# Kernel tuning notes

Hardware: AMD Instinct MI355X
Metric: run time of the kernel (lower is better)

The kernel has to match this reference:

```python
import jax, jax.numpy as jnp
import numpy as np

B, S, HID = 4, 2048, 1024
NH = 16
HD = HID // NH  # 64


def setup_inputs() -> dict:
    key = jax.random.key(0)
    k1, k2, k3 = jax.random.split(key, 3)
    x = jax.random.normal(k1, (B, S, HID), dtype=jnp.float32)
    # causal sparse mask: True = attend
    mask = jnp.tril(jnp.ones((S, S), dtype=bool))
    w_qkv = jax.random.normal(k2, (HID, 3 * HID), dtype=jnp.float32) * 0.02
    b_qkv = jnp.zeros((3 * HID,), dtype=jnp.float32)
    w_out = jax.random.normal(k3, (HID, HID), dtype=jnp.float32) * 0.02
    b_out = jnp.zeros((HID,), dtype=jnp.float32)
    return {"x": x, "mask": mask, "w_qkv": w_qkv, "b_qkv": b_qkv,
            "w_out": w_out, "b_out": b_out}


def reference(x, mask, w_qkv, b_qkv, w_out, b_out):
    bsz, seq_len, hid = x.shape
    # QKV projection -> [B, S, H, 3*D] -> [B, H, S, 3*D]
    qkv = (x @ w_qkv + b_qkv).reshape(bsz, seq_len, NH, 3 * HD).transpose(0, 2, 1, 3)
    q, k, v = jnp.split(qkv, 3, axis=-1)  # each [B, H, S, D]
    scale = 1.0 / jnp.sqrt(jnp.asarray(HD, dtype=x.dtype))
    scores = jnp.einsum('bhqd,bhkd->bhqk', q, k) * scale
    scores = jnp.where(mask[None, None, :, :], scores, jnp.asarray(-jnp.inf, dtype=scores.dtype))
    probs = jax.nn.softmax(scores, axis=-1)
    context = jnp.einsum('bhqk,bhkd->bhqd', probs, v)  # [B, H, S, D]
    context = context.transpose(0, 2, 1, 3).reshape(bsz, seq_len, hid)
    return context @ w_out + b_out
```

## Files before the change

kernel.cpp:

```cpp
#include <hip/hip_runtime.h>
#include <stdint.h>

#define S_LEN 2048
#define NHEAD 16
#define HDIM  64
#define HIDDEN 1024
#define BATCH 4

typedef float f32x4 __attribute__((ext_vector_type(4)));
typedef __bf16 bf16x8 __attribute__((ext_vector_type(8)));
typedef unsigned short u16;

union U4B8 { uint4 u; bf16x8 b; };

__device__ __forceinline__ bf16x8 as_b8(uint4 u){ U4B8 x; x.u = u; return x.b; }

__device__ __forceinline__ f32x4 mfma16(uint4 a, uint4 b, f32x4 c){
  return __builtin_amdgcn_mfma_f32_16x16x32_bf16(as_b8(a), as_b8(b), c, 0, 0, 0);
}

__device__ __forceinline__ u16 f2bf(float f){
  __bf16 h = (__bf16)f;
  return __builtin_bit_cast(u16, h);
}

__device__ __forceinline__ float exp2fast(float x){
  return __builtin_exp2f(x);
}

__device__ __forceinline__ void gload16(const void* g, void* l){
  __builtin_amdgcn_global_load_lds(
      (const __attribute__((address_space(1))) unsigned int*)g,
      (__attribute__((address_space(3))) unsigned int*)l, 16, 0, 0);
}

#define QSCALE 0.18033688f
#define DEFER_THR 11.5f

__global__ __launch_bounds__(256) void k_cvt(const float* __restrict__ in,
                                             u16* __restrict__ out, int n4){
  int i = blockIdx.x * 256 + threadIdx.x;
  int stride = gridDim.x * 256;
  for (; i < n4; i += stride){
    float4 v = ((const float4*)in)[i];
    unsigned lo = (unsigned)f2bf(v.x) | ((unsigned)f2bf(v.y) << 16);
    unsigned hi = (unsigned)f2bf(v.z) | ((unsigned)f2bf(v.w) << 16);
    ((uint2*)out)[i] = make_uint2(lo, hi);
  }
}

__global__ __launch_bounds__(256) void k_transpose(const float* __restrict__ in,
                                                   u16* __restrict__ out,
                                                   int K, int N){
  __shared__ float t[32][33];
  int tx = threadIdx.x & 31, ty = threadIdx.x >> 5;
  int n0 = blockIdx.x * 32, k0 = blockIdx.y * 32;
  #pragma unroll
  for (int i = 0; i < 4; ++i)
    t[ty + i*8][tx] = in[(size_t)(k0 + ty + i*8) * N + n0 + tx];
  __syncthreads();
  #pragma unroll
  for (int i = 0; i < 4; ++i)
    out[(size_t)(n0 + ty + i*8) * K + k0 + tx] = f2bf(t[tx][ty + i*8]);
}

__device__ __forceinline__ void stage_gemm(
    const u16* __restrict__ A, const u16* __restrict__ Bt,
    u16* As, u16* Bs, int row0, int col0, int K, int k0, int wave, int lane)
{
  #pragma unroll
  for (int p = 0; p < 2; ++p){
    int chunk = wave * 128 + p * 64 + lane;
    int r = chunk >> 2, cseg = chunk & 3;
    const u16* ga = A  + (size_t)(row0 + r) * K + k0 + cseg * 8;
    gload16(ga, As + (size_t)(wave * 128 + p * 64) * 8);
    const u16* gb = Bt + (size_t)(col0 + r) * K + k0 + cseg * 8;
    gload16(gb, Bs + (size_t)(wave * 128 + p * 64) * 8);
  }
}

template<int MODE>
__global__ __launch_bounds__(256) void k_gemm(
    const u16* __restrict__ A, const u16* __restrict__ Bt,
    const float* __restrict__ bias,
    u16* __restrict__ oq, u16* __restrict__ ok, u16* __restrict__ ov,
    float* __restrict__ of, int M, int N, int K)
{
  __shared__ u16 As[2][128 * 32];
  __shared__ u16 Bs[2][128 * 32];
  const int tid  = threadIdx.x;
  const int wave = tid >> 6, lane = tid & 63;
  const int l4 = lane >> 4, lm = lane & 15;
  const int wr = wave >> 1, wc = wave & 1;
  const int row0 = blockIdx.y * 128;
  const int col0 = blockIdx.x * 128;

  const f32x4 fzero = {0.f, 0.f, 0.f, 0.f};
  f32x4 acc[4][4];
  #pragma unroll
  for (int m = 0; m < 4; ++m)
    #pragma unroll
    for (int n = 0; n < 4; ++n) acc[m][n] = fzero;

  stage_gemm(A, Bt, &As[0][0], &Bs[0][0], row0, col0, K, 0, wave, lane);

  const int nks = K >> 5;
  #pragma unroll 1
  for (int ks = 0; ks < nks; ++ks){
    const int cur = ks & 1;
    if (ks + 1 < nks){
      stage_gemm(A, Bt, &As[cur ^ 1][0], &Bs[cur ^ 1][0],
                 row0, col0, K, (ks + 1) << 5, wave, lane);
      asm volatile("s_waitcnt vmcnt(4)" ::: "memory");
    } else {
      asm volatile("s_waitcnt vmcnt(0)" ::: "memory");
    }
    __builtin_amdgcn_s_barrier();
    asm volatile("" ::: "memory");

    uint4 af[4], bf[4];
    #pragma unroll
    for (int m = 0; m < 4; ++m)
      af[m] = *(const uint4*)&As[cur][(wr * 64 + m * 16 + lm) * 32 + l4 * 8];
    #pragma unroll
    for (int n = 0; n < 4; ++n)
      bf[n] = *(const uint4*)&Bs[cur][(wc * 64 + n * 16 + lm) * 32 + l4 * 8];
    __builtin_amdgcn_s_setprio(1);
    #pragma unroll
    for (int m = 0; m < 4; ++m)
      #pragma unroll
      for (int n = 0; n < 4; ++n)
        acc[m][n] = mfma16(af[m], bf[n], acc[m][n]);
    __builtin_amdgcn_s_setprio(0);

    asm volatile("" ::: "memory");
    __builtin_amdgcn_s_barrier();
    asm volatile("" ::: "memory");
  }

  #pragma unroll
  for (int m = 0; m < 4; ++m){
    #pragma unroll
    for (int n = 0; n < 4; ++n){
      int c = col0 + wc * 64 + n * 16 + lm;
      float bv = bias[c];
      #pragma unroll
      for (int r = 0; r < 4; ++r){
        int row = row0 + wr * 64 + m * 16 + l4 * 4 + r;
        float val = acc[m][n][r] + bv;
        if (MODE == 0){
          int h = c / 192, e = c % 192;
          int which = e >> 6, d = e & 63;
          int b = row >> 11, s = row & 2047;
          int bh = b * 16 + h;
          if (which == 2){
            ov[((size_t)bh * HDIM + d) * S_LEN + s] = f2bf(val);
          } else {
            if (which == 0) val *= QSCALE;
            size_t idx = ((size_t)bh * S_LEN + s) * HDIM + d;
            u16* dst = (which == 0) ? oq : ok;
            dst[idx] = f2bf(val);
          }
        } else {
          of[(size_t)row * N + c] = val;
        }
      }
    }
  }
}

__device__ __forceinline__ void stage_tile(
    const u16* __restrict__ kB, const u16* __restrict__ vB,
    u16* ldsK, u16* ldsV, int kbase, int wave, int lane)
{
  #pragma unroll
  for (int p = 0; p < 2; ++p){
    int ch  = wave * 128 + p * 64 + lane;
    int row = ch >> 3;
    int cc  = (ch & 7) << 4;
    int sc  = cc ^ ((row & 7) << 4);
    const u16* gk = kB + (size_t)(kbase + row) * HDIM + (sc >> 1);
    gload16(gk, ldsK + (size_t)(wave * 128 + p * 64) * 8);
    const u16* gv = vB + (size_t)row * S_LEN + kbase + (sc >> 1);
    gload16(gv, ldsV + (size_t)(wave * 128 + p * 64) * 8);
  }
}

__global__ __launch_bounds__(256) void k_attn(
    const u16* __restrict__ q, const u16* __restrict__ kk,
    const u16* __restrict__ vt, u16* __restrict__ ctx)
{
  __shared__ u16 KV[2][2][64 * 64];
  __shared__ u16 Ps[4][2][16][72];

  const int bid = blockIdx.x;
  const int bh = bid & 63;
  const int pr = bid >> 6;
  const int wave = threadIdx.x >> 6, lane = threadIdx.x & 63;
  const int l4 = lane >> 4, lm = lane & 15;
  const size_t base = (size_t)bh * (S_LEN * HDIM);
  const u16* kB = kk + base;
  const u16* vB = vt + base;
  const int b = bh >> 4, h = bh & 15;
  const f32x4 fz = {0.f, 0.f, 0.f, 0.f};

  #pragma unroll 1
  for (int half = 0; half < 2; ++half){
    const int st = half ? (15 - pr) : pr;
    const int q0 = st * 128 + wave * 32;

    uint4 qf[2][2];
    #pragma unroll
    for (int f = 0; f < 2; ++f){
      const u16* qr = q + base + (size_t)(q0 + f * 16 + lm) * HDIM + l4 * 8;
      qf[f][0] = *(const uint4*)qr;
      qf[f][1] = *(const uint4*)(qr + 32);
    }

    float mr[2] = {-1e30f, -1e30f}, lsp[2] = {0.f, 0.f};
    f32x4 acc[2][4];
    #pragma unroll
    for (int f = 0; f < 2; ++f)
      #pragma unroll
      for (int tt = 0; tt < 4; ++tt) acc[f][tt] = fz;

    const int nkt = 2 * st + 2;

    stage_tile(kB, vB, &KV[0][0][0], &KV[0][1][0], 0, wave, lane);

    #pragma unroll 1
    for (int kt = 0; kt < nkt; ++kt){
      const int cur = kt & 1;
      const int kbase = kt << 6;
      if (kt + 1 < nkt){
        stage_tile(kB, vB, &KV[cur ^ 1][0][0], &KV[cur ^ 1][1][0],
                   (kt + 1) << 6, wave, lane);
        asm volatile("s_waitcnt vmcnt(4)" ::: "memory");
      } else {
        asm volatile("s_waitcnt vmcnt(0)" ::: "memory");
      }
      __builtin_amdgcn_s_barrier();
      asm volatile("" ::: "memory");

      if (kbase < q0 + 32){
        const u16* ldsK = &KV[cur][0][0];
        const u16* ldsV = &KV[cur][1][0];

        f32x4 sv[2][4];
        __builtin_amdgcn_s_setprio(1);
        #pragma unroll
        for (int g = 0; g < 4; ++g){
          int rk = g * 16 + lm;
          int xa = (l4 * 16) ^ ((rk & 7) << 4);
          int xb = (64 + l4 * 16) ^ ((rk & 7) << 4);
          const u16* krow = ldsK + rk * 64;
          uint4 kf0 = *(const uint4*)(krow + (xa >> 1));
          uint4 kf1 = *(const uint4*)(krow + (xb >> 1));
          sv[0][g] = mfma16(kf0, qf[0][0], fz);
          sv[0][g] = mfma16(kf1, qf[0][1], sv[0][g]);
          sv[1][g] = mfma16(kf0, qf[1][0], fz);
          sv[1][g] = mfma16(kf1, qf[1][1], sv[1][g]);
        }
        __builtin_amdgcn_s_setprio(0);

        const bool tail = (kbase + 63 > q0);

        #pragma unroll
        for (int f = 0; f < 2; ++f){
          if (tail){
            #pragma unroll
            for (int g = 0; g < 4; ++g)
              #pragma unroll
              for (int r = 0; r < 4; ++r){
                int kg = kbase + g * 16 + l4 * 4 + r;
                int qg = q0 + f * 16 + lm;
                if (kg > qg) sv[f][g][r] = -1e30f;
              }
          }

          float pm = sv[f][0][0];
          #pragma unroll
          for (int g = 0; g < 4; ++g)
            #pragma unroll
            for (int r = 0; r < 4; ++r) pm = fmaxf(pm, sv[f][g][r]);
          pm = fmaxf(pm, __shfl_xor(pm, 16));
          pm = fmaxf(pm, __shfl_xor(pm, 32));

          if (__any(pm > mr[f] + DEFER_THR)){
            float mn = fmaxf(mr[f], pm);
            float corr = exp2fast(mr[f] - mn);
            mr[f] = mn;
            lsp[f] *= corr;
            float cf[4];
            #pragma unroll
            for (int r = 0; r < 4; ++r) cf[r] = __shfl(corr, l4 * 4 + r);
            #pragma unroll
            for (int tt = 0; tt < 4; ++tt)
              #pragma unroll
              for (int r = 0; r < 4; ++r) acc[f][tt][r] *= cf[r];
          }

          float s_ = 0.f;
          #pragma unroll
          for (int g = 0; g < 4; ++g){
            float p0 = exp2fast(sv[f][g][0] - mr[f]);
            float p1 = exp2fast(sv[f][g][1] - mr[f]);
            float p2 = exp2fast(sv[f][g][2] - mr[f]);
            float p3 = exp2fast(sv[f][g][3] - mr[f]);
            s_ += (p0 + p1) + (p2 + p3);
            uint2 w;
            w.x = (unsigned)f2bf(p0) | ((unsigned)f2bf(p1) << 16);
            w.y = (unsigned)f2bf(p2) | ((unsigned)f2bf(p3) << 16);
            *(uint2*)&Ps[wave][f][lm][g * 16 + l4 * 4] = w;
          }
          lsp[f] += s_;
        }

        __builtin_amdgcn_wave_barrier();
        uint4 pa[2][2];
        #pragma unroll
        for (int f = 0; f < 2; ++f){
          pa[f][0] = *(const uint4*)&Ps[wave][f][lm][l4 * 8];
          pa[f][1] = *(const uint4*)&Ps[wave][f][lm][32 + l4 * 8];
        }

        __builtin_amdgcn_s_setprio(1);
        #pragma unroll
        for (int tt = 0; tt < 4; ++tt){
          int rv = tt * 16 + lm;
          int xa = (l4 * 16) ^ ((rv & 7) << 4);
          int xb = (64 + l4 * 16) ^ ((rv & 7) << 4);
          const u16* vrow = ldsV + rv * 64;
          uint4 v0 = *(const uint4*)(vrow + (xa >> 1));
          uint4 v1 = *(const uint4*)(vrow + (xb >> 1));
          acc[0][tt] = mfma16(pa[0][0], v0, acc[0][tt]);
          acc[0][tt] = mfma16(pa[0][1], v1, acc[0][tt]);
          acc[1][tt] = mfma16(pa[1][0], v0, acc[1][tt]);
          acc[1][tt] = mfma16(pa[1][1], v1, acc[1][tt]);
        }
        __builtin_amdgcn_s_setprio(0);
      }

      asm volatile("" ::: "memory");
      __builtin_amdgcn_s_barrier();
      asm volatile("" ::: "memory");
    }

    #pragma unroll
    for (int f = 0; f < 2; ++f){
      lsp[f] += __shfl_xor(lsp[f], 16);
      lsp[f] += __shfl_xor(lsp[f], 32);
      float inv_ = 1.0f / lsp[f];
      float ivr[4];
      #pragma unroll
      for (int r = 0; r < 4; ++r) ivr[r] = __shfl(inv_, l4 * 4 + r);
      #pragma unroll
      for (int tt = 0; tt < 4; ++tt)
        #pragma unroll
        for (int r = 0; r < 4; ++r){
          int srow = q0 + f * 16 + l4 * 4 + r;
          float val = acc[f][tt][r] * ivr[r];
          ctx[((size_t)b * S_LEN + srow) * HIDDEN + h * HDIM + tt * 16 + lm] = f2bf(val);
        }
    }
  }
}

extern "C" void kernel_launch(void* const* d_in, const int* in_sizes, int n_in,
                              void* d_out, int out_size, void* d_ws, size_t ws_size,
                              hipStream_t stream)
{
  const float* x     = (const float*)d_in[0];
  const float* w_qkv = (const float*)d_in[2];
  const float* b_qkv = (const float*)d_in[3];
  const float* w_out = (const float*)d_in[4];
  const float* b_out = (const float*)d_in[5];

  char* ws = (char*)d_ws;
  u16* xbf   = (u16*)(ws);
  u16* wqkvT = (u16*)(ws + 16777216);
  u16* woutT = (u16*)(ws + 23068672);
  u16* qb    = (u16*)(ws + 25165824);
  u16* kb    = (u16*)(ws + 41943040);
  u16* vb    = (u16*)(ws + 58720256);

  k_cvt<<<2048, 256, 0, stream>>>(x, xbf, (BATCH * S_LEN * HIDDEN) / 4);
  k_transpose<<<dim3(96, 32), 256, 0, stream>>>(w_qkv, wqkvT, HIDDEN, 3 * HIDDEN);
  k_transpose<<<dim3(32, 32), 256, 0, stream>>>(w_out, woutT, HIDDEN, HIDDEN);
  k_gemm<0><<<dim3(24, 64), 256, 0, stream>>>(xbf, wqkvT, b_qkv,
                                              qb, kb, vb, nullptr,
                                              BATCH * S_LEN, 3 * HIDDEN, HIDDEN);
  k_attn<<<512, 256, 0, stream>>>(qb, kb, vb, xbf);
  k_gemm<1><<<dim3(8, 64), 256, 0, stream>>>(xbf, woutT, b_out,
                                             nullptr, nullptr, nullptr,
                                             (float*)d_out, BATCH * S_LEN, HIDDEN, HIDDEN);
}
```

Measured before the change: 218.3 us.

## Triple-buffer and swizzle GEMM LDS, remap blocks per XCD, widen attention blocks

The GEMM moves to a three-stage LDS pipeline with an XOR swizzle on the 32-element K segments, which is meant to reduce bank conflicts and keep more loads in flight. It also remaps the 1D block index so neighbouring tiles land on the same XCD, aiming for better L2 reuse. The attention kernel goes to 512-thread blocks covering 256 query rows, so each staged K/V tile is shared by eight waves instead of four. The row-max shuffle reduction is now done only when the deferred-rescale check fires. The extra buffer raises LDS use, and the larger attention blocks halve the block count, which risks load imbalance on the causal mask.

```diff
diff --git a/kernel.cpp b/kernel.cpp
--- a/kernel.cpp
+++ b/kernel.cpp
@@ -36,6 +36,9 @@
 
 #define QSCALE 0.18033688f
 #define DEFER_THR 11.5f
+
+#define FENCE asm volatile("" ::: "memory")
+#define PH_BAR do{ FENCE; __builtin_amdgcn_s_barrier(); FENCE; }while(0)
 
 __global__ __launch_bounds__(256) void k_cvt(const float* __restrict__ in,
                                              u16* __restrict__ out, int n4){
@@ -72,9 +75,10 @@
   for (int p = 0; p < 2; ++p){
     int chunk = wave * 128 + p * 64 + lane;
     int r = chunk >> 2, cseg = chunk & 3;
-    const u16* ga = A  + (size_t)(row0 + r) * K + k0 + cseg * 8;
+    int sseg = cseg ^ (r & 3);
+    const u16* ga = A  + (size_t)(row0 + r) * K + k0 + sseg * 8;
     gload16(ga, As + (size_t)(wave * 128 + p * 64) * 8);
-    const u16* gb = Bt + (size_t)(col0 + r) * K + k0 + cseg * 8;
+    const u16* gb = Bt + (size_t)(col0 + r) * K + k0 + sseg * 8;
     gload16(gb, Bs + (size_t)(wave * 128 + p * 64) * 8);
   }
 }
@@ -84,16 +88,23 @@
     const u16* __restrict__ A, const u16* __restrict__ Bt,
     const float* __restrict__ bias,
     u16* __restrict__ oq, u16* __restrict__ ok, u16* __restrict__ ov,
-    float* __restrict__ of, int M, int N, int K)
+    float* __restrict__ of, int M, int N, int K, int nx)
 {
-  __shared__ u16 As[2][128 * 32];
-  __shared__ u16 Bs[2][128 * 32];
+  __shared__ u16 As[3][128 * 32];
+  __shared__ u16 Bs[3][128 * 32];
   const int tid  = threadIdx.x;
   const int wave = tid >> 6, lane = tid & 63;
   const int l4 = lane >> 4, lm = lane & 15;
   const int wr = wave >> 1, wc = wave & 1;
-  const int row0 = blockIdx.y * 128;
-  const int col0 = blockIdx.x * 128;
+
+  const int bid = blockIdx.x;
+  const int nwg = gridDim.x;
+  const int ny8 = nwg / (8 * nx);
+  const int xcd = bid & 7, t = bid >> 3;
+  const int by = xcd * ny8 + t / nx;
+  const int bx = t % nx;
+  const int row0 = by * 128;
+  const int col0 = bx * 128;
 
   const f32x4 fzero = {0.f, 0.f, 0.f, 0.f};
   f32x4 acc[4][4];
@@ -102,29 +113,36 @@
     #pragma unroll
     for (int n = 0; n < 4; ++n) acc[m][n] = fzero;
 
+  const int nks = K >> 5;
   stage_gemm(A, Bt, &As[0][0], &Bs[0][0], row0, col0, K, 0, wave, lane);
-
-  const int nks = K >> 5;
+  stage_gemm(A, Bt, &As[1][0], &Bs[1][0], row0, col0, K, 32, wave, lane);
+
+  int cur = 0;
   #pragma unroll 1
   for (int ks = 0; ks < nks; ++ks){
-    const int cur = ks & 1;
-    if (ks + 1 < nks){
-      stage_gemm(A, Bt, &As[cur ^ 1][0], &Bs[cur ^ 1][0],
-                 row0, col0, K, (ks + 1) << 5, wave, lane);
+    if (ks + 2 < nks){
+      int nxt = cur + 2; if (nxt >= 3) nxt -= 3;
+      stage_gemm(A, Bt, &As[nxt][0], &Bs[nxt][0],
+                 row0, col0, K, (ks + 2) << 5, wave, lane);
+      asm volatile("s_waitcnt vmcnt(8)" ::: "memory");
+    } else if (ks + 1 < nks){
       asm volatile("s_waitcnt vmcnt(4)" ::: "memory");
     } else {
       asm volatile("s_waitcnt vmcnt(0)" ::: "memory");
     }
-    __builtin_amdgcn_s_barrier();
-    asm volatile("" ::: "memory");
+    PH_BAR;
 
     uint4 af[4], bf[4];
     #pragma unroll
-    for (int m = 0; m < 4; ++m)
-      af[m] = *(const uint4*)&As[cur][(wr * 64 + m * 16 + lm) * 32 + l4 * 8];
-    #pragma unroll
-    for (int n = 0; n < 4; ++n)
-      bf[n] = *(const uint4*)&Bs[cur][(wc * 64 + n * 16 + lm) * 32 + l4 * 8];
+    for (int m = 0; m < 4; ++m){
+      int rr = wr * 64 + m * 16 + lm;
+      af[m] = *(const uint4*)&As[cur][rr * 32 + (l4 ^ (rr & 3)) * 8];
+    }
+    #pragma unroll
+    for (int n = 0; n < 4; ++n){
+      int rr = wc * 64 + n * 16 + lm;
+      bf[n] = *(const uint4*)&Bs[cur][rr * 32 + (l4 ^ (rr & 3)) * 8];
+    }
     __builtin_amdgcn_s_setprio(1);
     #pragma unroll
     for (int m = 0; m < 4; ++m)
@@ -133,9 +151,9 @@
         acc[m][n] = mfma16(af[m], bf[n], acc[m][n]);
     __builtin_amdgcn_s_setprio(0);
 
-    asm volatile("" ::: "memory");
-    __builtin_amdgcn_s_barrier();
-    asm volatile("" ::: "memory");
+    PH_BAR;
+
+    cur = cur + 1; if (cur >= 3) cur -= 3;
   }
 
   #pragma unroll
@@ -169,29 +187,24 @@
   }
 }
 
-__device__ __forceinline__ void stage_tile(
+__device__ __forceinline__ void stage_tile8(
     const u16* __restrict__ kB, const u16* __restrict__ vB,
     u16* ldsK, u16* ldsV, int kbase, int wave, int lane)
 {
-  #pragma unroll
-  for (int p = 0; p < 2; ++p){
-    int ch  = wave * 128 + p * 64 + lane;
-    int row = ch >> 3;
-    int cc  = (ch & 7) << 4;
-    int sc  = cc ^ ((row & 7) << 4);
-    const u16* gk = kB + (size_t)(kbase + row) * HDIM + (sc >> 1);
-    gload16(gk, ldsK + (size_t)(wave * 128 + p * 64) * 8);
-    const u16* gv = vB + (size_t)row * S_LEN + kbase + (sc >> 1);
-    gload16(gv, ldsV + (size_t)(wave * 128 + p * 64) * 8);
-  }
-}
-
-__global__ __launch_bounds__(256) void k_attn(
+  int ch  = wave * 64 + lane;
+  int row = ch >> 3;
+  int cc  = (ch & 7) << 4;
+  int sc  = cc ^ ((row & 7) << 4);
+  gload16(kB + (size_t)(kbase + row) * HDIM + (sc >> 1), ldsK + (size_t)wave * 512);
+  gload16(vB + (size_t)row * S_LEN + kbase + (sc >> 1), ldsV + (size_t)wave * 512);
+}
+
+__global__ __launch_bounds__(512, 4) void k_attn(
     const u16* __restrict__ q, const u16* __restrict__ kk,
     const u16* __restrict__ vt, u16* __restrict__ ctx)
 {
   __shared__ u16 KV[2][2][64 * 64];
-  __shared__ u16 Ps[4][2][16][72];
+  __shared__ u16 Ps[8][2][16][72];
 
   const int bid = blockIdx.x;
   const int bh = bid & 63;
@@ -206,8 +219,8 @@
 
   #pragma unroll 1
   for (int half = 0; half < 2; ++half){
-    const int st = half ? (15 - pr) : pr;
-    const int q0 = st * 128 + wave * 32;
+    const int st = half ? (7 - pr) : pr;
+    const int q0 = st * 256 + wave * 32;
 
     uint4 qf[2][2];
     #pragma unroll
@@ -224,23 +237,22 @@
       #pragma unroll
       for (int tt = 0; tt < 4; ++tt) acc[f][tt] = fz;
 
-    const int nkt = 2 * st + 2;
-
-    stage_tile(kB, vB, &KV[0][0][0], &KV[0][1][0], 0, wave, lane);
+    const int nkt = 4 * st + 4;
+
+    stage_tile8(kB, vB, &KV[0][0][0], &KV[0][1][0], 0, wave, lane);
 
     #pragma unroll 1
     for (int kt = 0; kt < nkt; ++kt){
       const int cur = kt & 1;
       const int kbase = kt << 6;
       if (kt + 1 < nkt){
-        stage_tile(kB, vB, &KV[cur ^ 1][0][0], &KV[cur ^ 1][1][0],
-                   (kt + 1) << 6, wave, lane);
-        asm volatile("s_waitcnt vmcnt(4)" ::: "memory");
+        stage_tile8(kB, vB, &KV[cur ^ 1][0][0], &KV[cur ^ 1][1][0],
+                    (kt + 1) << 6, wave, lane);
+        asm volatile("s_waitcnt vmcnt(2)" ::: "memory");
       } else {
         asm volatile("s_waitcnt vmcnt(0)" ::: "memory");
       }
-      __builtin_amdgcn_s_barrier();
-      asm volatile("" ::: "memory");
+      PH_BAR;
 
       if (kbase < q0 + 32){
         const u16* ldsK = &KV[cur][0][0];
@@ -278,15 +290,15 @@
               }
           }
 
-          float pm = sv[f][0][0];
+          float pml = sv[f][0][0];
           #pragma unroll
           for (int g = 0; g < 4; ++g)
             #pragma unroll
-            for (int r = 0; r < 4; ++r) pm = fmaxf(pm, sv[f][g][r]);
-          pm = fmaxf(pm, __shfl_xor(pm, 16));
-          pm = fmaxf(pm, __shfl_xor(pm, 32));
-
-          if (__any(pm > mr[f] + DEFER_THR)){
+            for (int r = 0; r < 4; ++r) pml = fmaxf(pml, sv[f][g][r]);
+
+          if (__any(pml > mr[f] + DEFER_THR)){
+            float pm = fmaxf(pml, __shfl_xor(pml, 16));
+            pm = fmaxf(pm, __shfl_xor(pm, 32));
             float mn = fmaxf(mr[f], pm);
             float corr = exp2fast(mr[f] - mn);
             mr[f] = mn;
@@ -341,9 +353,7 @@
         __builtin_amdgcn_s_setprio(0);
       }
 
-      asm volatile("" ::: "memory");
-      __builtin_amdgcn_s_barrier();
-      asm volatile("" ::: "memory");
+      PH_BAR;
     }
 
     #pragma unroll
@@ -387,11 +397,11 @@
   k_cvt<<<2048, 256, 0, stream>>>(x, xbf, (BATCH * S_LEN * HIDDEN) / 4);
   k_transpose<<<dim3(96, 32), 256, 0, stream>>>(w_qkv, wqkvT, HIDDEN, 3 * HIDDEN);
   k_transpose<<<dim3(32, 32), 256, 0, stream>>>(w_out, woutT, HIDDEN, HIDDEN);
-  k_gemm<0><<<dim3(24, 64), 256, 0, stream>>>(xbf, wqkvT, b_qkv,
-                                              qb, kb, vb, nullptr,
-                                              BATCH * S_LEN, 3 * HIDDEN, HIDDEN);
-  k_attn<<<512, 256, 0, stream>>>(qb, kb, vb, xbf);
-  k_gemm<1><<<dim3(8, 64), 256, 0, stream>>>(xbf, woutT, b_out,
-                                             nullptr, nullptr, nullptr,
-                                             (float*)d_out, BATCH * S_LEN, HIDDEN, HIDDEN);
-}
+  k_gemm<0><<<24 * 64, 256, 0, stream>>>(xbf, wqkvT, b_qkv,
+                                         qb, kb, vb, nullptr,
+                                         BATCH * S_LEN, 3 * HIDDEN, HIDDEN, 24);
+  k_attn<<<256, 512, 0, stream>>>(qb, kb, vb, xbf);
+  k_gemm<1><<<8 * 64, 256, 0, stream>>>(xbf, woutT, b_out,
+                                        nullptr, nullptr, nullptr,
+                                        (float*)d_out, BATCH * S_LEN, HIDDEN, HIDDEN, 8);
+}
```

Measured after the change: 207.5 us. 1.05x faster.
